# Kernel tuning notes

Measured on AMD Instinct MI355X. Metric: run time of the kernel, lower is better.

Reference implementation:

```python
import jax, jax.numpy as jnp
import numpy as np

N, D, H = 6144, 768, 3
DH = D // H

def _lrelu(v):
    return jnp.where(v >= 0, v, 0.2 * v)

def setup_inputs() -> dict:
    key = jax.random.key(0)
    ks = jax.random.split(key, 8)
    s = 1.0 / np.sqrt(D)  # xavier-ish scale for D->D linears
    return {
        "x": jax.random.normal(ks[0], (N, D), dtype=jnp.float32),
        "adj_matrix": jax.random.randint(ks[1], (N, N), 0, 2, dtype=jnp.int32),
        "W_fc": jax.random.normal(ks[2], (D, D), dtype=jnp.float32) * s,
        "b_fc": jnp.zeros((D,), dtype=jnp.float32),
        "W_qfc": jax.random.normal(ks[3], (D, D), dtype=jnp.float32) * s,
        "b_qfc": jnp.zeros((D,), dtype=jnp.float32),
        "W_final": jax.random.normal(ks[4], (D, D), dtype=jnp.float32) * s,
        "b_final": jnp.zeros((D,), dtype=jnp.float32),
    }

def reference(x, adj_matrix, W_fc, b_fc, W_qfc, b_qfc, W_final, b_final):
    # x: [N, D], adj_matrix: [N, N] (0/1). Dropout is identity at eval.
    x_new = _lrelu(x @ W_fc.T + b_fc)          # [N, D]
    q = _lrelu(x_new @ W_qfc.T + b_qfc)        # [N, D]
    # torch.split(dim=2) into 3 contiguous chunks then cat on dim 0 == reshape heads
    xh = x_new.reshape(N, H, DH).transpose(1, 0, 2)   # [3, N, DH]
    qh = q.reshape(N, H, DH).transpose(1, 0, 2)       # [3, N, DH]
    scores = jnp.einsum('hnd,hmd->hnm', qh, xh) / 10.0  # [3, N, N]
    mask = (adj_matrix == 0)[None, :, :]                 # [1, N, N] -> broadcast
    scores = jnp.where(mask, -jnp.inf, scores)
    attn = jax.nn.softmax(scores, axis=-1)               # [3, N, N]
    out = jnp.einsum('hnm,hmd->hnd', attn, xh)           # [3, N, DH]
    out = out.transpose(1, 0, 2).reshape(N, D)           # cat heads on feature dim
    out = x + out                                        # residual 1
    ret = x + _lrelu(out @ W_final.T + b_final)          # residual 2
    return ret
```

## Files before the change

### kernel.cpp

```cpp
#include <hip/hip_runtime.h>
#include <stdint.h>

#define N_TOK 6144
#define DMODEL 768
#define NHEAD 3
#define DHEAD 256
#define NWORDS (N_TOK/32)
#define NT NWORDS

typedef __bf16 bf16x8 __attribute__((ext_vector_type(8)));
typedef float f32x4 __attribute__((ext_vector_type(4)));
typedef unsigned short u16;
typedef u16 u16x8 __attribute__((ext_vector_type(8)));
typedef u16 u16x4 __attribute__((ext_vector_type(4)));
typedef unsigned int u32;

__device__ __forceinline__ u16 f2bf(float f) {
  __bf16 b = (__bf16)f;
  return __builtin_bit_cast(u16, b);
}
__device__ __forceinline__ float bf2f(u16 u) {
  union { u32 u; float f; } v; v.u = (u32)u << 16; return v.f;
}
__device__ __forceinline__ float lrelu(float v) { return v >= 0.f ? v : 0.2f * v; }

__global__ __launch_bounds__(256) void pack_adj(const int* __restrict__ adj,
                                                u32* __restrict__ bits) {
  size_t wid = (size_t)blockIdx.x * 256 + threadIdx.x;
  const int4* p = reinterpret_cast<const int4*>(adj + wid * 32);
  u32 m = 0;
#pragma unroll
  for (int i = 0; i < 8; ++i) {
    int4 v = p[i];
    m |= (v.x != 0 ? 1u : 0u) << (i * 4 + 0);
    m |= (v.y != 0 ? 1u : 0u) << (i * 4 + 1);
    m |= (v.z != 0 ? 1u : 0u) << (i * 4 + 2);
    m |= (v.w != 0 ? 1u : 0u) << (i * 4 + 3);
  }
  bits[wid] = m;
}

__global__ __launch_bounds__(256) void transpose_bf(const u16* __restrict__ src,
                                                    u16* __restrict__ dst) {
  __shared__ u16 t[64][72];
  const int n0 = blockIdx.x * 64, d0 = blockIdx.y * 64;
  const int tid = threadIdx.x;
#pragma unroll
  for (int i = 0; i < 2; ++i) {
    int c = tid + i * 256;
    int r = c >> 3, c8 = (c & 7) * 8;
    *reinterpret_cast<u16x8*>(&t[r][c8]) =
        *reinterpret_cast<const u16x8*>(src + (size_t)(n0 + r) * DMODEL + d0 + c8);
  }
  __syncthreads();
#pragma unroll
  for (int i = 0; i < 2; ++i) {
    int c = tid + i * 256;
    int dr = c >> 3, n8 = (c & 7) * 8;
    u16x8 v;
#pragma unroll
    for (int j = 0; j < 8; ++j) v[j] = t[n8 + j][dr];
    *reinterpret_cast<u16x8*>(dst + (size_t)(d0 + dr) * N_TOK + n0 + n8) = v;
  }
}

__global__ void init_knmax(u32* knmax2) {
  if (threadIdx.x < NHEAD) knmax2[threadIdx.x] = 0;
}

__global__ __launch_bounds__(256) void knorm_max(const u16* __restrict__ xnew,
                                                 u32* __restrict__ knmax2) {
  int n = blockIdx.x * 256 + threadIdx.x;
  int h = blockIdx.y;
  const u16* row = xnew + (size_t)n * DMODEL + h * DHEAD;
  float s = 0.f;
#pragma unroll 4
  for (int i = 0; i < 32; ++i) {
    u16x8 v = *reinterpret_cast<const u16x8*>(row + i * 8);
#pragma unroll
    for (int j = 0; j < 8; ++j) { float f = bf2f(v[j]); s += f * f; }
  }
#pragma unroll
  for (int off = 1; off < 64; off <<= 1) s = fmaxf(s, __shfl_xor(s, off));
  if ((threadIdx.x & 63) == 0) atomicMax(knmax2 + h, __float_as_uint(s));
}

__global__ __launch_bounds__(256) void qbound(const u16* __restrict__ qbf,
                                              const u32* __restrict__ knmax2,
                                              float* __restrict__ Mrow) {
  int n = blockIdx.x * 256 + threadIdx.x;
  int h = blockIdx.y;
  const u16* row = qbf + (size_t)n * DMODEL + h * DHEAD;
  float s = 0.f;
#pragma unroll 4
  for (int i = 0; i < 32; ++i) {
    u16x8 v = *reinterpret_cast<const u16x8*>(row + i * 8);
#pragma unroll
    for (int j = 0; j < 8; ++j) { float f = bf2f(v[j]); s += f * f; }
  }
  float kn2 = __uint_as_float(knmax2[h]);
  Mrow[(size_t)h * N_TOK + n] = sqrtf(s * kn2);
}

template <int ABF, int FINAL>
__global__ __launch_bounds__(256) void gemm_nt(const void* __restrict__ Aptr,
                                               const float* __restrict__ W,
                                               const float* __restrict__ bias,
                                               const float* __restrict__ resid,
                                               u16* __restrict__ out_bf,
                                               float* __restrict__ out_f,
                                               float oscale) {
  __shared__ u16 As[64][72];
  __shared__ u16 Bs[128][72];
  const int tid = threadIdx.x;
  const int w = tid >> 6, lane = tid & 63, lr = lane & 15, lg = lane >> 4;
  const int m0 = blockIdx.x * 64, n0 = blockIdx.y * 128;
  const int wr = (w >> 1) * 32, wc = (w & 1) * 64;
  f32x4 acc[2][4] = {};
  for (int kt = 0; kt < DMODEL / 64; ++kt) {
    __syncthreads();
#pragma unroll
    for (int i = 0; i < 2; ++i) {
      int c = tid + i * 256;
      int row = c >> 3, c8 = (c & 7) * 8;
      int gcol = kt * 64 + c8;
      if (ABF) {
        *reinterpret_cast<u16x8*>(&As[row][c8]) = *reinterpret_cast<const u16x8*>(
            (const u16*)Aptr + (size_t)(m0 + row) * DMODEL + gcol);
      } else {
        const float* src = (const float*)Aptr + (size_t)(m0 + row) * DMODEL + gcol;
        float4 f0 = *reinterpret_cast<const float4*>(src);
        float4 f1 = *reinterpret_cast<const float4*>(src + 4);
        u16x8 v = {f2bf(f0.x), f2bf(f0.y), f2bf(f0.z), f2bf(f0.w),
                   f2bf(f1.x), f2bf(f1.y), f2bf(f1.z), f2bf(f1.w)};
        *reinterpret_cast<u16x8*>(&As[row][c8]) = v;
      }
    }
#pragma unroll
    for (int i = 0; i < 4; ++i) {
      int c = tid + i * 256;
      int row = c >> 3, c8 = (c & 7) * 8;
      int gcol = kt * 64 + c8;
      const float* wsrc = W + (size_t)(n0 + row) * DMODEL + gcol;
      float4 g0 = *reinterpret_cast<const float4*>(wsrc);
      float4 g1 = *reinterpret_cast<const float4*>(wsrc + 4);
      u16x8 wv = {f2bf(g0.x), f2bf(g0.y), f2bf(g0.z), f2bf(g0.w),
                  f2bf(g1.x), f2bf(g1.y), f2bf(g1.z), f2bf(g1.w)};
      *reinterpret_cast<u16x8*>(&Bs[row][c8]) = wv;
    }
    __syncthreads();
#pragma unroll
    for (int ks = 0; ks < 2; ++ks) {
      bf16x8 a[2], b[4];
#pragma unroll
      for (int mi = 0; mi < 2; ++mi)
        a[mi] = *reinterpret_cast<const bf16x8*>(&As[wr + mi * 16 + lr][ks * 32 + lg * 8]);
#pragma unroll
      for (int ni = 0; ni < 4; ++ni)
        b[ni] = *reinterpret_cast<const bf16x8*>(&Bs[wc + ni * 16 + lr][ks * 32 + lg * 8]);
#pragma unroll
      for (int mi = 0; mi < 2; ++mi)
#pragma unroll
        for (int ni = 0; ni < 4; ++ni)
          acc[mi][ni] =
              __builtin_amdgcn_mfma_f32_16x16x32_bf16(a[mi], b[ni], acc[mi][ni], 0, 0, 0);
    }
  }
#pragma unroll
  for (int mi = 0; mi < 2; ++mi)
#pragma unroll
    for (int ni = 0; ni < 4; ++ni)
#pragma unroll
      for (int r = 0; r < 4; ++r) {
        int grow = m0 + wr + mi * 16 + lg * 4 + r;
        int gcol = n0 + wc + ni * 16 + lr;
        float v = lrelu(acc[mi][ni][r] + bias[gcol]);
        size_t idx = (size_t)grow * DMODEL + gcol;
        if (FINAL)
          out_f[idx] = resid[idx] + v;
        else
          out_bf[idx] = f2bf(v * oscale);
      }
}

template <int SPLIT>
__global__ __launch_bounds__(256) void attn_fused(
    const u16* __restrict__ Kmat,
    const u16* __restrict__ Qmat,
    const u16* __restrict__ VT,
    const u32* __restrict__ bits,
    const float* __restrict__ Mrow,
    const float* __restrict__ x,
    u16* __restrict__ out2,
    float* __restrict__ Opart,
    float* __restrict__ lpart) {
  __shared__ u16 Ks[32][264];
  __shared__ u16 Vs[256][36];
  __shared__ u16 Ps[4][16][40];
  __shared__ float lss[64];
  const int tid = threadIdx.x;
  const int w = tid >> 6, lane = tid & 63, lr = lane & 15, lg = lane >> 4;
  const int q0 = blockIdx.x * 64;
  const int h = blockIdx.y;
  const int z = blockIdx.z;
  const int qrow = q0 + w * 16 + lr;
  const int qp = (w >> 1) * 2;
  const int dbase = (w & 1) * 8;

  bf16x8 qf[8];
  {
    const u16* qrowp = Qmat + (size_t)qrow * DMODEL + h * DHEAD + lg * 8;
#pragma unroll
    for (int s = 0; s < 8; ++s) qf[s] = *reinterpret_cast<const bf16x8*>(qrowp + s * 32);
  }
  const float Mr = Mrow[(size_t)h * N_TOK + qrow];
  f32x4 o[2][8] = {};
  float lsum = 0.f;

  const int t0 = z * (NT / SPLIT), t1 = t0 + NT / SPLIT;

  u16x8 kst[4], vst[4];
  u32 wnext, wcur;

  auto issue_tile = [&](int kt) {
#pragma unroll
    for (int i = 0; i < 4; ++i) {
      int c = tid + i * 256;
      int kr = c >> 5, kc = (c & 31) * 8;
      kst[i] = *reinterpret_cast<const u16x8*>(
          Kmat + (size_t)(kt * 32 + kr) * DMODEL + h * DHEAD + kc);
      int vr = c >> 2, vc = (c & 3) * 8;
      vst[i] = *reinterpret_cast<const u16x8*>(
          VT + (size_t)(h * DHEAD + vr) * N_TOK + kt * 32 + vc);
    }
    wnext = bits[(size_t)qrow * NWORDS + kt];
  };
  auto write_tile = [&]() {
#pragma unroll
    for (int i = 0; i < 4; ++i) {
      int c = tid + i * 256;
      int kr = c >> 5, kc = (c & 31) * 8;
      *reinterpret_cast<u16x8*>(&Ks[kr][kc]) = kst[i];
      int vr = c >> 2, vc = (c & 3) * 8;
      *reinterpret_cast<u16x8*>(&Vs[vr][vc]) = vst[i];
    }
  };

  issue_tile(t0);

  for (int kt = t0; kt < t1; ++kt) {
    __syncthreads();
    write_tile();
    wcur = wnext;
    if (kt + 1 < t1) issue_tile(kt + 1);
    __syncthreads();

    f32x4 st[2] = {};
#pragma unroll
    for (int s = 0; s < 8; ++s) {
      bf16x8 k0 = *reinterpret_cast<const bf16x8*>(&Ks[lr][s * 32 + lg * 8]);
      bf16x8 k1 = *reinterpret_cast<const bf16x8*>(&Ks[16 + lr][s * 32 + lg * 8]);
      st[0] = __builtin_amdgcn_mfma_f32_16x16x32_bf16(k0, qf[s], st[0], 0, 0, 0);
      st[1] = __builtin_amdgcn_mfma_f32_16x16x32_bf16(k1, qf[s], st[1], 0, 0, 0);
    }
#pragma unroll
    for (int kb = 0; kb < 2; ++kb) {
      u16x4 pk;
#pragma unroll
      for (int r = 0; r < 4; ++r) {
        int keyl = kb * 16 + lg * 4 + r;
        float pe = ((wcur >> keyl) & 1u) ? __expf(st[kb][r] - Mr) : 0.f;
        lsum += pe;
        pk[r] = f2bf(pe);
      }
      *reinterpret_cast<u16x4*>(&Ps[w][lr][kb * 16 + lg * 4]) = pk;
    }
    __syncthreads();

    bf16x8 pf0 = *reinterpret_cast<const bf16x8*>(&Ps[qp][lr][lg * 8]);
    bf16x8 pf1 = *reinterpret_cast<const bf16x8*>(&Ps[qp + 1][lr][lg * 8]);
#pragma unroll
    for (int d = 0; d < 8; ++d) {
      bf16x8 vf = *reinterpret_cast<const bf16x8*>(&Vs[(dbase + d) * 16 + lr][lg * 8]);
      o[0][d] = __builtin_amdgcn_mfma_f32_16x16x32_bf16(pf0, vf, o[0][d], 0, 0, 0);
      o[1][d] = __builtin_amdgcn_mfma_f32_16x16x32_bf16(pf1, vf, o[1][d], 0, 0, 0);
    }
  }

  lsum += __shfl_xor(lsum, 16);
  lsum += __shfl_xor(lsum, 32);

  if (SPLIT == 1) {
    if (lane < 16) lss[w * 16 + lr] = lsum;
    __syncthreads();
#pragma unroll
    for (int t = 0; t < 2; ++t)
#pragma unroll
      for (int d = 0; d < 8; ++d)
#pragma unroll
        for (int r = 0; r < 4; ++r) {
          int grow = q0 + (w >> 1) * 32 + t * 16 + lg * 4 + r;
          int gcol = h * DHEAD + (w & 1) * 128 + d * 16 + lr;
          size_t idx = (size_t)grow * DMODEL + gcol;
          float ls = lss[(w >> 1) * 32 + t * 16 + lg * 4 + r];
          out2[idx] = f2bf(x[idx] + o[t][d][r] / ls);
        }
  } else {
    float* Op = Opart + (size_t)z * N_TOK * DMODEL;
#pragma unroll
    for (int t = 0; t < 2; ++t)
#pragma unroll
      for (int d = 0; d < 8; ++d)
#pragma unroll
        for (int r = 0; r < 4; ++r) {
          int grow = q0 + (w >> 1) * 32 + t * 16 + lg * 4 + r;
          int gcol = h * DHEAD + (w & 1) * 128 + d * 16 + lr;
          Op[(size_t)grow * DMODEL + gcol] = o[t][d][r];
        }
    if (lane < 16)
      lpart[((size_t)z * NHEAD + h) * N_TOK + qrow] = lsum;
  }
}

template <int SPLIT>
__global__ __launch_bounds__(256) void attn_combine(const float* __restrict__ Opart,
                                                    const float* __restrict__ lpart,
                                                    const float* __restrict__ x,
                                                    u16* __restrict__ out2) {
  int g = blockIdx.x * 256 + threadIdx.x;
  int q = g / (DMODEL / 4);
  int col = (g % (DMODEL / 4)) * 4;
  int h = col >> 8;
  float L = 0.f;
#pragma unroll
  for (int s = 0; s < SPLIT; ++s)
    L += lpart[((size_t)s * NHEAD + h) * N_TOK + q];
  float rL = 1.f / L;
  size_t idx = (size_t)q * DMODEL + col;
  float4 acc = make_float4(0.f, 0.f, 0.f, 0.f);
#pragma unroll
  for (int s = 0; s < SPLIT; ++s) {
    float4 O = *reinterpret_cast<const float4*>(Opart + (size_t)s * N_TOK * DMODEL + idx);
    acc.x += O.x; acc.y += O.y; acc.z += O.z; acc.w += O.w;
  }
  float4 xv = *reinterpret_cast<const float4*>(x + idx);
  u16x4 r;
  r[0] = f2bf(xv.x + acc.x * rL);
  r[1] = f2bf(xv.y + acc.y * rL);
  r[2] = f2bf(xv.z + acc.z * rL);
  r[3] = f2bf(xv.w + acc.w * rL);
  *reinterpret_cast<u16x4*>(out2 + idx) = r;
}

extern "C" void kernel_launch(void* const* d_in, const int* in_sizes, int n_in,
                              void* d_out, int out_size, void* d_ws, size_t ws_size,
                              hipStream_t stream) {
  const float* x     = (const float*)d_in[0];
  const int*   adj   = (const int*)d_in[1];
  const float* W_fc  = (const float*)d_in[2];
  const float* b_fc  = (const float*)d_in[3];
  const float* W_qfc = (const float*)d_in[4];
  const float* b_qfc = (const float*)d_in[5];
  const float* W_fin = (const float*)d_in[6];
  const float* b_fin = (const float*)d_in[7];
  float* out = (float*)d_out;

  char* ws = (char*)d_ws;
  size_t off = 0;
  auto alloc = [&](size_t bytes) {
    char* p = ws + off;
    off += (bytes + 255) & ~(size_t)255;
    return p;
  };
  u16* xnew_bf = (u16*)alloc((size_t)N_TOK * DMODEL * 2);
  u16* q_bf    = (u16*)alloc((size_t)N_TOK * DMODEL * 2);
  u16* xT      = (u16*)alloc((size_t)DMODEL * N_TOK * 2);
  u16* out2_bf = (u16*)alloc((size_t)N_TOK * DMODEL * 2);
  u32* bits    = (u32*)alloc((size_t)N_TOK * NWORDS * 4);
  u32* knmax2  = (u32*)alloc(NHEAD * 4);
  float* Mrow  = (float*)alloc((size_t)NHEAD * N_TOK * 4);
  size_t base_off = off;
  float* Opart = (float*)alloc((size_t)6 * N_TOK * DMODEL * 4);
  float* lpart = (float*)alloc((size_t)6 * NHEAD * N_TOK * 4);
  size_t need6 = off;
  auto needN = [&](size_t n) {
    return base_off + (((size_t)n * N_TOK * DMODEL * 4 + 255) & ~(size_t)255) +
           (((size_t)n * NHEAD * N_TOK * 4 + 255) & ~(size_t)255);
  };
  const int split = (ws_size >= need6) ? 6
                  : (ws_size >= needN(4)) ? 4
                  : (ws_size >= needN(2)) ? 2 : 1;

  pack_adj<<<N_TOK * NWORDS / 256, 256, 0, stream>>>(adj, bits);
  dim3 ggrid(N_TOK / 64, DMODEL / 128);
  gemm_nt<0, 0><<<ggrid, 256, 0, stream>>>(x, W_fc, b_fc, nullptr, xnew_bf, nullptr, 1.0f);
  gemm_nt<1, 0><<<ggrid, 256, 0, stream>>>(xnew_bf, W_qfc, b_qfc, nullptr, q_bf, nullptr,
                                           0.1f);
  transpose_bf<<<dim3(N_TOK / 64, DMODEL / 64), 256, 0, stream>>>(xnew_bf, xT);
  init_knmax<<<1, 64, 0, stream>>>(knmax2);
  dim3 bgrid(N_TOK / 256, NHEAD);
  knorm_max<<<bgrid, 256, 0, stream>>>(xnew_bf, knmax2);
  qbound<<<bgrid, 256, 0, stream>>>(q_bf, knmax2, Mrow);
  dim3 cgrid(N_TOK * DMODEL / 4 / 256);
  if (split == 6) {
    attn_fused<6><<<dim3(N_TOK / 64, NHEAD, 6), 256, 0, stream>>>(
        xnew_bf, q_bf, xT, bits, Mrow, x, out2_bf, Opart, lpart);
    attn_combine<6><<<cgrid, 256, 0, stream>>>(Opart, lpart, x, out2_bf);
  } else if (split == 4) {
    attn_fused<4><<<dim3(N_TOK / 64, NHEAD, 4), 256, 0, stream>>>(
        xnew_bf, q_bf, xT, bits, Mrow, x, out2_bf, Opart, lpart);
    attn_combine<4><<<cgrid, 256, 0, stream>>>(Opart, lpart, x, out2_bf);
  } else if (split == 2) {
    attn_fused<2><<<dim3(N_TOK / 64, NHEAD, 2), 256, 0, stream>>>(
        xnew_bf, q_bf, xT, bits, Mrow, x, out2_bf, Opart, lpart);
    attn_combine<2><<<cgrid, 256, 0, stream>>>(Opart, lpart, x, out2_bf);
  } else {
    attn_fused<1><<<dim3(N_TOK / 64, NHEAD, 1), 256, 0, stream>>>(
        xnew_bf, q_bf, xT, bits, Mrow, x, out2_bf, Opart, lpart);
  }
  gemm_nt<1, 1><<<ggrid, 256, 0, stream>>>(out2_bf, W_fin, b_fin, x, nullptr, out, 1.0f);
}
```

Before: 385.8 us.

## Pre-convert GEMM operands to bf16 and use larger register-prefetched tiles

Adds a conversion kernel that turns x and the three weight matrices into bf16 once, so the GEMMs no longer convert fp32 to bf16 inside their inner loop. The GEMM tile grows from 64x128 to 128x128 with a 4x4 MFMA accumulator per wave, and the next K tile is prefetched into registers while the current one is computed. The aim is to cut repeated weight conversion and global traffic in the three linear layers, at the cost of four extra launches, more workspace, and fewer blocks per GEMM. The attention kernel, which likely dominates the runtime, is unchanged.

```diff
diff --git a/kernel.cpp b/kernel.cpp
--- a/kernel.cpp
+++ b/kernel.cpp
@@ -23,6 +23,16 @@
   union { u32 u; float f; } v; v.u = (u32)u << 16; return v.f;
 }
 __device__ __forceinline__ float lrelu(float v) { return v >= 0.f ? v : 0.2f * v; }
+
+__global__ __launch_bounds__(256) void cvt_bf(const float* __restrict__ src,
+                                              u16* __restrict__ dst) {
+  size_t i = ((size_t)blockIdx.x * 256 + threadIdx.x) * 8;
+  float4 a = *reinterpret_cast<const float4*>(src + i);
+  float4 b = *reinterpret_cast<const float4*>(src + i + 4);
+  u16x8 v = {f2bf(a.x), f2bf(a.y), f2bf(a.z), f2bf(a.w),
+             f2bf(b.x), f2bf(b.y), f2bf(b.z), f2bf(b.w)};
+  *reinterpret_cast<u16x8*>(dst + i) = v;
+}
 
 __global__ __launch_bounds__(256) void pack_adj(const int* __restrict__ adj,
                                                 u32* __restrict__ bits) {
@@ -102,64 +112,58 @@
   Mrow[(size_t)h * N_TOK + n] = sqrtf(s * kn2);
 }
 
-template <int ABF, int FINAL>
-__global__ __launch_bounds__(256) void gemm_nt(const void* __restrict__ Aptr,
-                                               const float* __restrict__ W,
+template <int FINAL>
+__global__ __launch_bounds__(256) void gemm_bf(const u16* __restrict__ A,
+                                               const u16* __restrict__ W,
                                                const float* __restrict__ bias,
                                                const float* __restrict__ resid,
                                                u16* __restrict__ out_bf,
                                                float* __restrict__ out_f,
                                                float oscale) {
-  __shared__ u16 As[64][72];
+  __shared__ u16 As[128][72];
   __shared__ u16 Bs[128][72];
   const int tid = threadIdx.x;
   const int w = tid >> 6, lane = tid & 63, lr = lane & 15, lg = lane >> 4;
-  const int m0 = blockIdx.x * 64, n0 = blockIdx.y * 128;
-  const int wr = (w >> 1) * 32, wc = (w & 1) * 64;
-  f32x4 acc[2][4] = {};
+  const int m0 = blockIdx.x * 128, n0 = blockIdx.y * 128;
+  const int wr = (w >> 1) * 64, wc = (w & 1) * 64;
+  f32x4 acc[4][4] = {};
+  u16x8 ast[4], bst[4];
+  const int row = tid >> 3, c8 = (tid & 7) * 8;
+
+  auto issue_tile = [&](int kt) {
+#pragma unroll
+    for (int i = 0; i < 4; ++i) {
+      int r = row + i * 32;
+      ast[i] = *reinterpret_cast<const u16x8*>(A + (size_t)(m0 + r) * DMODEL + kt * 64 + c8);
+      bst[i] = *reinterpret_cast<const u16x8*>(W + (size_t)(n0 + r) * DMODEL + kt * 64 + c8);
+    }
+  };
+  auto write_tile = [&]() {
+#pragma unroll
+    for (int i = 0; i < 4; ++i) {
+      int r = row + i * 32;
+      *reinterpret_cast<u16x8*>(&As[r][c8]) = ast[i];
+      *reinterpret_cast<u16x8*>(&Bs[r][c8]) = bst[i];
+    }
+  };
+
+  issue_tile(0);
   for (int kt = 0; kt < DMODEL / 64; ++kt) {
     __syncthreads();
-#pragma unroll
-    for (int i = 0; i < 2; ++i) {
-      int c = tid + i * 256;
-      int row = c >> 3, c8 = (c & 7) * 8;
-      int gcol = kt * 64 + c8;
-      if (ABF) {
-        *reinterpret_cast<u16x8*>(&As[row][c8]) = *reinterpret_cast<const u16x8*>(
-            (const u16*)Aptr + (size_t)(m0 + row) * DMODEL + gcol);
-      } else {
-        const float* src = (const float*)Aptr + (size_t)(m0 + row) * DMODEL + gcol;
-        float4 f0 = *reinterpret_cast<const float4*>(src);
-        float4 f1 = *reinterpret_cast<const float4*>(src + 4);
-        u16x8 v = {f2bf(f0.x), f2bf(f0.y), f2bf(f0.z), f2bf(f0.w),
-                   f2bf(f1.x), f2bf(f1.y), f2bf(f1.z), f2bf(f1.w)};
-        *reinterpret_cast<u16x8*>(&As[row][c8]) = v;
-      }
-    }
-#pragma unroll
-    for (int i = 0; i < 4; ++i) {
-      int c = tid + i * 256;
-      int row = c >> 3, c8 = (c & 7) * 8;
-      int gcol = kt * 64 + c8;
-      const float* wsrc = W + (size_t)(n0 + row) * DMODEL + gcol;
-      float4 g0 = *reinterpret_cast<const float4*>(wsrc);
-      float4 g1 = *reinterpret_cast<const float4*>(wsrc + 4);
-      u16x8 wv = {f2bf(g0.x), f2bf(g0.y), f2bf(g0.z), f2bf(g0.w),
-                  f2bf(g1.x), f2bf(g1.y), f2bf(g1.z), f2bf(g1.w)};
-      *reinterpret_cast<u16x8*>(&Bs[row][c8]) = wv;
-    }
+    write_tile();
+    if (kt + 1 < DMODEL / 64) issue_tile(kt + 1);
     __syncthreads();
 #pragma unroll
     for (int ks = 0; ks < 2; ++ks) {
-      bf16x8 a[2], b[4];
-#pragma unroll
-      for (int mi = 0; mi < 2; ++mi)
+      bf16x8 a[4], b[4];
+#pragma unroll
+      for (int mi = 0; mi < 4; ++mi)
         a[mi] = *reinterpret_cast<const bf16x8*>(&As[wr + mi * 16 + lr][ks * 32 + lg * 8]);
 #pragma unroll
       for (int ni = 0; ni < 4; ++ni)
         b[ni] = *reinterpret_cast<const bf16x8*>(&Bs[wc + ni * 16 + lr][ks * 32 + lg * 8]);
 #pragma unroll
-      for (int mi = 0; mi < 2; ++mi)
+      for (int mi = 0; mi < 4; ++mi)
 #pragma unroll
         for (int ni = 0; ni < 4; ++ni)
           acc[mi][ni] =
@@ -167,7 +171,7 @@
     }
   }
 #pragma unroll
-  for (int mi = 0; mi < 2; ++mi)
+  for (int mi = 0; mi < 4; ++mi)
 #pragma unroll
     for (int ni = 0; ni < 4; ++ni)
 #pragma unroll
@@ -376,6 +380,10 @@
   u16* q_bf    = (u16*)alloc((size_t)N_TOK * DMODEL * 2);
   u16* xT      = (u16*)alloc((size_t)DMODEL * N_TOK * 2);
   u16* out2_bf = (u16*)alloc((size_t)N_TOK * DMODEL * 2);
+  u16* x_bf    = (u16*)alloc((size_t)N_TOK * DMODEL * 2);
+  u16* wfc_bf  = (u16*)alloc((size_t)DMODEL * DMODEL * 2);
+  u16* wqf_bf  = (u16*)alloc((size_t)DMODEL * DMODEL * 2);
+  u16* wfi_bf  = (u16*)alloc((size_t)DMODEL * DMODEL * 2);
   u32* bits    = (u32*)alloc((size_t)N_TOK * NWORDS * 4);
   u32* knmax2  = (u32*)alloc(NHEAD * 4);
   float* Mrow  = (float*)alloc((size_t)NHEAD * N_TOK * 4);
@@ -391,11 +399,16 @@
                   : (ws_size >= needN(4)) ? 4
                   : (ws_size >= needN(2)) ? 2 : 1;
 
+  cvt_bf<<<N_TOK * DMODEL / 8 / 256, 256, 0, stream>>>(x, x_bf);
+  cvt_bf<<<DMODEL * DMODEL / 8 / 256, 256, 0, stream>>>(W_fc, wfc_bf);
+  cvt_bf<<<DMODEL * DMODEL / 8 / 256, 256, 0, stream>>>(W_qfc, wqf_bf);
+  cvt_bf<<<DMODEL * DMODEL / 8 / 256, 256, 0, stream>>>(W_fin, wfi_bf);
   pack_adj<<<N_TOK * NWORDS / 256, 256, 0, stream>>>(adj, bits);
-  dim3 ggrid(N_TOK / 64, DMODEL / 128);
-  gemm_nt<0, 0><<<ggrid, 256, 0, stream>>>(x, W_fc, b_fc, nullptr, xnew_bf, nullptr, 1.0f);
-  gemm_nt<1, 0><<<ggrid, 256, 0, stream>>>(xnew_bf, W_qfc, b_qfc, nullptr, q_bf, nullptr,
-                                           0.1f);
+
+  dim3 ggrid(N_TOK / 128, DMODEL / 128);
+  gemm_bf<0><<<ggrid, 256, 0, stream>>>(x_bf, wfc_bf, b_fc, nullptr, xnew_bf, nullptr, 1.0f);
+  gemm_bf<0><<<ggrid, 256, 0, stream>>>(xnew_bf, wqf_bf, b_qfc, nullptr, q_bf, nullptr,
+                                        0.1f);
   transpose_bf<<<dim3(N_TOK / 64, DMODEL / 64), 256, 0, stream>>>(xnew_bf, xT);
   init_knmax<<<1, 64, 0, stream>>>(knmax2);
   dim3 bgrid(N_TOK / 256, NHEAD);
@@ -418,5 +431,5 @@
     attn_fused<1><<<dim3(N_TOK / 64, NHEAD, 1), 256, 0, stream>>>(
         xnew_bf, q_bf, xT, bits, Mrow, x, out2_bf, Opart, lpart);
   }
-  gemm_nt<1, 1><<<ggrid, 256, 0, stream>>>(out2_bf, W_fin, b_fin, x, nullptr, out, 1.0f);
-}
+  gemm_bf<1><<<ggrid, 256, 0, stream>>>(out2_bf, wfi_bf, b_fin, x, nullptr, out, 1.0f);
+}
```

After: 340.8 us, median of 2. 1.13x faster.
